# Optimization experiments

Hardware: AMD Instinct MI355X
Metric: run time of the kernel (lower is better)

The kernel has to match this reference:

```python
import jax, jax.numpy as jnp
import numpy as np

N = 50000
E = 1600000
D_IN = 512
EPS = 1e-5


def setup_inputs() -> dict:
    key = jax.random.key(0)
    ks = jax.random.split(key, 20)
    p = lambda k, shape: jax.random.normal(k, shape, dtype=jnp.float32) * 0.05
    return {
        "x": jax.random.normal(ks[0], (N, D_IN), dtype=jnp.float32),
        "edge_index": jax.random.randint(ks[1], (2, E), 0, N),
        "edge_weight": jax.random.uniform(ks[2], (E,), dtype=jnp.float32),
        # conv1: ChebConv(512->400) with K=1,2,3 (weight per Chebyshev order)
        "W1a": p(ks[3], (1, D_IN, 400)), "b1a": p(ks[4], (400,)),
        "W1b": p(ks[5], (2, D_IN, 400)), "b1b": p(ks[6], (400,)),
        "W1c": p(ks[7], (3, D_IN, 400)), "b1c": p(ks[8], (400,)),
        "g1": jnp.ones((1200,), jnp.float32), "beta1": jnp.zeros((1200,), jnp.float32),
        # conv2: ChebConv(1200->100) with K=1,2,3
        "W2a": p(ks[9], (1, 1200, 100)), "b2a": p(ks[10], (100,)),
        "W2b": p(ks[11], (2, 1200, 100)), "b2b": p(ks[12], (100,)),
        "W2c": p(ks[13], (3, 1200, 100)), "b2c": p(ks[14], (100,)),
        "g2": jnp.ones((300,), jnp.float32), "beta2": jnp.zeros((300,), jnp.float32),
        "Wl": p(ks[15], (300, 10)), "bl": p(ks[16], (10,)),
    }


def _cheb(x, row, col, norm, W, b):
    """PyG ChebConv forward: out = sum_k T_k(L_hat) x @ W[k] + b.
    L_hat (sym norm, lambda_max=2) = -D^{-1/2} A D^{-1/2}, zero diagonal,
    applied as scatter: (L_hat h)[col] += norm_e * h[row]."""
    K = W.shape[0]
    n = x.shape[0]
    prop = lambda h: jax.ops.segment_sum(norm[:, None] * h[row], col, num_segments=n)
    out = x @ W[0]
    Tx_prev, Tx = x, None
    if K >= 2:
        Tx = prop(x)
        out = out + Tx @ W[1]
    for k in range(2, K):
        Tx_new = 2.0 * prop(Tx) - Tx_prev
        out = out + Tx_new @ W[k]
        Tx_prev, Tx = Tx, Tx_new
    return out + b


def _bn(h, g, beta):
    # BatchNorm over nodes (training-mode batch statistics, biased var)
    mu = h.mean(axis=0)
    var = h.var(axis=0)
    return (h - mu) * jax.lax.rsqrt(var + EPS) * g + beta


def reference(x, edge_index, edge_weight, W1a, b1a, W1b, b1b, W1c, b1c, g1, beta1,
              W2a, b2a, W2b, b2b, W2c, b2c, g2, beta2, Wl, bl):
    row, col = edge_index[0], edge_index[1]
    deg = jax.ops.segment_sum(edge_weight, row, num_segments=x.shape[0])
    safe = jnp.where(deg > 0, deg, 1.0)
    dis = jnp.where(deg > 0, jax.lax.rsqrt(safe), 0.0)  # deg^{-1/2}, inf -> 0
    norm = -dis[row] * edge_weight * dis[col]  # scaled-Laplacian edge weights

    h = jnp.concatenate([
        _cheb(x, row, col, norm, W1a, b1a),
        _cheb(x, row, col, norm, W1b, b1b),
        _cheb(x, row, col, norm, W1c, b1c)], axis=1)  # [N, 1200]
    h = jax.nn.relu(_bn(h, g1, beta1))

    h = jnp.concatenate([
        _cheb(h, row, col, norm, W2a, b2a),
        _cheb(h, row, col, norm, W2b, b2b),
        _cheb(h, row, col, norm, W2c, b2c)], axis=1)  # [N, 300]
    h = _bn(h, g2, beta2)

    logits = h @ Wl + bl  # [N, 10]
    return jax.nn.log_softmax(logits, axis=1)
```

## Files before the change

### kernel.cpp

```cpp
#include <hip/hip_runtime.h>
#include <math.h>

#define EPSB 1e-5f

typedef __attribute__((ext_vector_type(8))) short short8;
typedef __attribute__((ext_vector_type(4))) float floatx4;
typedef __attribute__((ext_vector_type(2))) float floatx2;

__device__ inline float bf2f(unsigned short h) {
  union { unsigned int u; float f; } v; v.u = ((unsigned int)h) << 16; return v.f;
}
__device__ inline unsigned short f2bf(float f) {
  union { float f; unsigned int u; } v; v.f = f;
  unsigned int r = v.u + 0x7fffu + ((v.u >> 16) & 1u);
  return (unsigned short)(r >> 16);
}

__device__ __forceinline__ void gl2lds16(const unsigned short* g, unsigned short* l) {
  __builtin_amdgcn_global_load_lds(
      (const __attribute__((address_space(1))) unsigned int*)g,
      (__attribute__((address_space(3))) unsigned int*)l, 16, 0, 0);
}

__device__ __forceinline__ void pk4(floatx2* a, uint4 g, floatx2 wv) {
  unsigned int u[4] = {g.x, g.y, g.z, g.w};
#pragma unroll
  for (int j = 0; j < 4; j++) {
    union { unsigned int q; float f; } lo, hi;
    lo.q = u[j] << 16;
    hi.q = u[j] & 0xffff0000u;
    floatx2 v; v[0] = lo.f; v[1] = hi.f;
    asm("v_pk_fma_f32 %0, %1, %2, %0" : "+v"(a[j]) : "v"(v), "v"(wv));
  }
}


__global__ void degcnt_kernel(const int* __restrict__ row, const int* __restrict__ col,
                              const float* __restrict__ ew,
                              float* __restrict__ deg, int* __restrict__ cnt, int E) {
  int e = blockIdx.x * blockDim.x + threadIdx.x;
  if (e < E) {
    atomicAdd(&deg[row[e]], ew[e]);
    atomicAdd(&cnt[col[e]], 1);
  }
}

__global__ void dis_kernel(float* deg, int n) {
  int i = blockIdx.x * blockDim.x + threadIdx.x;
  if (i < n) { float d = deg[i]; deg[i] = d > 0.f ? rsqrtf(d) : 0.f; }
}

__global__ __launch_bounds__(1024) void scan1_kernel(const int* __restrict__ cnt,
                                                     int* __restrict__ off,
                                                     int* __restrict__ bsum, int n) {
  __shared__ int buf[1024];
  int tid = threadIdx.x;
  int idx = blockIdx.x * 1024 + tid;
  int v = (idx < n) ? cnt[idx] : 0;
  buf[tid] = v;
  __syncthreads();
  for (int s = 1; s < 1024; s <<= 1) {
    int t = (tid >= s) ? buf[tid - s] : 0;
    __syncthreads();
    if (tid >= s) buf[tid] += t;
    __syncthreads();
  }
  if (idx < n) off[idx] = buf[tid] - v;
  if (tid == 1023) bsum[blockIdx.x] = buf[1023];
}

__global__ void scan2_kernel(int* __restrict__ bsum, int* __restrict__ off,
                             int nb, int n) {
  if (threadIdx.x == 0 && blockIdx.x == 0) {
    int run = 0;
    for (int k = 0; k < nb; k++) { int t = bsum[k]; bsum[k] = run; run += t; }
    off[n] = run;
  }
}

__global__ void scan3_kernel(int* __restrict__ off, const int* __restrict__ bsum, int n) {
  int i = blockIdx.x * blockDim.x + threadIdx.x;
  if (i < n) off[i] += bsum[i >> 10];
}

__global__ void copy_kernel(const int* __restrict__ src, int* __restrict__ dst, int n) {
  int i = blockIdx.x * blockDim.x + threadIdx.x;
  if (i < n) dst[i] = src[i];
}

__global__ void fill_kernel(const int* __restrict__ row, const int* __restrict__ col,
                            const float* __restrict__ ew, const float* __restrict__ dis,
                            int* __restrict__ wptr,
                            int2* __restrict__ ePack, int E) {
  int e = blockIdx.x * blockDim.x + threadIdx.x;
  if (e < E) {
    int r = row[e], c = col[e];
    int p = atomicAdd(&wptr[c], 1);
    float nv = -dis[r] * ew[e] * dis[c];
    ePack[p] = make_int2(r, __float_as_int(nv));
  }
}


__global__ void cast_x_kernel(const float* __restrict__ x, unsigned short* __restrict__ xb,
                              int N) {
  int idx = blockIdx.x * blockDim.x + threadIdx.x;
  if (idx >= N * 128) return;
  int row = idx >> 7, c4 = idx & 127;
  float4 v = *reinterpret_cast<const float4*>(x + (size_t)row * 512 + c4 * 4);
  union { unsigned int u[2]; } p;
  p.u[0] = (unsigned int)f2bf(v.x) | ((unsigned int)f2bf(v.y) << 16);
  p.u[1] = (unsigned int)f2bf(v.z) | ((unsigned int)f2bf(v.w) << 16);
  *reinterpret_cast<uint2*>(xb + (size_t)row * 1536 + c4 * 4) = make_uint2(p.u[0], p.u[1]);
}

__global__ void wprep_kernel(const float* __restrict__ W, unsigned short* __restrict__ Bt,
                             int Ktot, int Nout, int ldBt, int rowOff) {
  int idx = blockIdx.x * blockDim.x + threadIdx.x;
  if (idx >= Ktot * Nout) return;
  int k = idx / Nout, n = idx - k * Nout;
  Bt[(size_t)(rowOff + n) * ldBt + k] = f2bf(W[idx]);
}

__global__ void padzero_kernel(unsigned short* __restrict__ h, int N) {
  int i = blockIdx.x * blockDim.x + threadIdx.x;
  if (i >= N * 2) return;
  *reinterpret_cast<uint4*>(h + (size_t)(i >> 1) * 1216 + 1200 + (i & 1) * 8) =
      make_uint4(0, 0, 0, 0);
}

__global__ void bcat_kernel(const float* __restrict__ a, const float* __restrict__ b,
                            const float* __restrict__ c, float* __restrict__ dst) {
  int i = threadIdx.x;
  if (i < 100) dst[i] = a[i];
  else if (i < 200) dst[i] = b[i - 100];
  else if (i < 300) dst[i] = c[i - 200];
}

__global__ __launch_bounds__(256) void prop_chunk_kernel(
    unsigned short* __restrict__ base, int ld,
    int srcCol, int dstCol, int subCol,
    const int* __restrict__ off, const int2* __restrict__ ePack,
    float scale, int N) {
  int chunk = blockIdx.x & 7;
  int g = blockIdx.x >> 3;
  int tid = threadIdx.x;
  int slot = (tid >> 3) & 3;
  int c8 = tid & 7;
  int v = g * 8 + (tid >> 5);
  bool valid = v < N;
  int vv = valid ? v : N - 1;
  int co = chunk * 64 + c8 * 8;
  const unsigned short* src = base + srcCol + co;
  int s = off[vv], e = off[vv + 1];
  int len = e - s;
  int s0 = s + (len * slot >> 2);
  int e0 = s + (len * (slot + 1) >> 2);
  floatx2 a2[4] = {}, b2[4] = {};
  int i = s0;
  for (; i + 3 < e0; i += 4) {
    int2 p0 = ePack[i];
    int2 p1 = ePack[i + 1];
    int2 p2 = ePack[i + 2];
    int2 p3 = ePack[i + 3];
    uint4 g0 = *reinterpret_cast<const uint4*>(src + (size_t)p0.x * ld);
    uint4 g1 = *reinterpret_cast<const uint4*>(src + (size_t)p1.x * ld);
    uint4 g2 = *reinterpret_cast<const uint4*>(src + (size_t)p2.x * ld);
    uint4 g3 = *reinterpret_cast<const uint4*>(src + (size_t)p3.x * ld);
    floatx2 w0; w0[0] = w0[1] = __int_as_float(p0.y);
    floatx2 w1; w1[0] = w1[1] = __int_as_float(p1.y);
    floatx2 w2; w2[0] = w2[1] = __int_as_float(p2.y);
    floatx2 w3; w3[0] = w3[1] = __int_as_float(p3.y);
    pk4(a2, g0, w0);
    pk4(b2, g1, w1);
    pk4(a2, g2, w2);
    pk4(b2, g3, w3);
  }
  for (; i < e0; i++) {
    int2 p = ePack[i];
    uint4 gg = *reinterpret_cast<const uint4*>(src + (size_t)p.x * ld);
    floatx2 wv; wv[0] = wv[1] = __int_as_float(p.y);
    pk4(a2, gg, wv);
  }
  float a[8];
#pragma unroll
  for (int j = 0; j < 4; j++) {
    a[2 * j]     = a2[j][0] + b2[j][0];
    a[2 * j + 1] = a2[j][1] + b2[j][1];
  }
#pragma unroll
  for (int j = 0; j < 8; j++) {
    a[j] += __shfl_xor(a[j], 8);
    a[j] += __shfl_xor(a[j], 16);
  }
  if (slot != 0 || !valid) return;
  if (subCol >= 0) {
    uint4 sv = *reinterpret_cast<const uint4*>(base + subCol + co + (size_t)v * ld);
    a[0] = scale * a[0] - bf2f((unsigned short)(sv.x & 0xffff));
    a[1] = scale * a[1] - bf2f((unsigned short)(sv.x >> 16));
    a[2] = scale * a[2] - bf2f((unsigned short)(sv.y & 0xffff));
    a[3] = scale * a[3] - bf2f((unsigned short)(sv.y >> 16));
    a[4] = scale * a[4] - bf2f((unsigned short)(sv.z & 0xffff));
    a[5] = scale * a[5] - bf2f((unsigned short)(sv.z >> 16));
    a[6] = scale * a[6] - bf2f((unsigned short)(sv.w & 0xffff));
    a[7] = scale * a[7] - bf2f((unsigned short)(sv.w >> 16));
  }
  uint4 o;
  o.x = (unsigned int)f2bf(a[0]) | ((unsigned int)f2bf(a[1]) << 16);
  o.y = (unsigned int)f2bf(a[2]) | ((unsigned int)f2bf(a[3]) << 16);
  o.z = (unsigned int)f2bf(a[4]) | ((unsigned int)f2bf(a[5]) << 16);
  o.w = (unsigned int)f2bf(a[6]) | ((unsigned int)f2bf(a[7]) << 16);
  *reinterpret_cast<uint4*>(base + dstCol + co + (size_t)v * ld) = o;
}

__global__ void prop_z_kernel(const unsigned short* __restrict__ Zcat,
                              const int* __restrict__ off, const int2* __restrict__ ePack,
                              float* __restrict__ h2f, unsigned short* __restrict__ U1) {
  int v = blockIdx.x;
  int f8 = threadIdx.x;
  if (f8 >= 38) return;
  int s = off[v], e = off[v + 1];
  floatx2 a2[4] = {}, b2[4] = {};
  int i = s;
  for (; i + 3 < e; i += 4) {
    int2 p0 = ePack[i];
    int2 p1 = ePack[i + 1];
    int2 p2 = ePack[i + 2];
    int2 p3 = ePack[i + 3];
    uint4 g0 = *reinterpret_cast<const uint4*>(Zcat + (size_t)p0.x * 304 + f8 * 8);
    uint4 g1 = *reinterpret_cast<const uint4*>(Zcat + (size_t)p1.x * 304 + f8 * 8);
    uint4 g2 = *reinterpret_cast<const uint4*>(Zcat + (size_t)p2.x * 304 + f8 * 8);
    uint4 g3 = *reinterpret_cast<const uint4*>(Zcat + (size_t)p3.x * 304 + f8 * 8);
    floatx2 w0; w0[0] = w0[1] = __int_as_float(p0.y);
    floatx2 w1; w1[0] = w1[1] = __int_as_float(p1.y);
    floatx2 w2; w2[0] = w2[1] = __int_as_float(p2.y);
    floatx2 w3; w3[0] = w3[1] = __int_as_float(p3.y);
    pk4(a2, g0, w0);
    pk4(b2, g1, w1);
    pk4(a2, g2, w2);
    pk4(b2, g3, w3);
  }
  for (; i < e; i++) {
    int2 p = ePack[i];
    uint4 raw = *reinterpret_cast<const uint4*>(Zcat + (size_t)p.x * 304 + f8 * 8);
    floatx2 wv; wv[0] = wv[1] = __int_as_float(p.y);
    pk4(a2, raw, wv);
  }
  float a[8];
#pragma unroll
  for (int j = 0; j < 4; j++) {
    a[2 * j]     = a2[j][0] + b2[j][0];
    a[2 * j + 1] = a2[j][1] + b2[j][1];
  }
  if (f8 < 25) {
    float* p = h2f + (size_t)v * 300 + 100 + f8 * 8;
#pragma unroll
    for (int j = 0; j < 8; j++) p[j] += a[j];
  } else {
    uint4 o;
    o.x = (unsigned int)f2bf(a[0]) | ((unsigned int)f2bf(a[1]) << 16);
    o.y = (unsigned int)f2bf(a[2]) | ((unsigned int)f2bf(a[3]) << 16);
    o.z = (unsigned int)f2bf(a[4]) | ((unsigned int)f2bf(a[5]) << 16);
    o.w = (unsigned int)f2bf(a[6]) | ((unsigned int)f2bf(a[7]) << 16);
    *reinterpret_cast<uint4*>(U1 + (size_t)v * 104 + (f8 - 25) * 8) = o;
  }
}

__global__ void prop_u_kernel(const unsigned short* __restrict__ U1,
                              const int* __restrict__ off, const int2* __restrict__ ePack,
                              const unsigned short* __restrict__ Zcat,
                              float* __restrict__ h2f) {
  int v = blockIdx.x;
  int f8 = threadIdx.x;
  if (f8 >= 13) return;
  int s = off[v], e = off[v + 1];
  floatx2 a2[4] = {}, b2[4] = {};
  int i = s;
  for (; i + 3 < e; i += 4) {
    int2 p0 = ePack[i];
    int2 p1 = ePack[i + 1];
    int2 p2 = ePack[i + 2];
    int2 p3 = ePack[i + 3];
    uint4 g0 = *reinterpret_cast<const uint4*>(U1 + (size_t)p0.x * 104 + f8 * 8);
    uint4 g1 = *reinterpret_cast<const uint4*>(U1 + (size_t)p1.x * 104 + f8 * 8);
    uint4 g2 = *reinterpret_cast<const uint4*>(U1 + (size_t)p2.x * 104 + f8 * 8);
    uint4 g3 = *reinterpret_cast<const uint4*>(U1 + (size_t)p3.x * 104 + f8 * 8);
    floatx2 w0; w0[0] = w0[1] = __int_as_float(p0.y);
    floatx2 w1; w1[0] = w1[1] = __int_as_float(p1.y);
    floatx2 w2; w2[0] = w2[1] = __int_as_float(p2.y);
    floatx2 w3; w3[0] = w3[1] = __int_as_float(p3.y);
    pk4(a2, g0, w0);
    pk4(b2, g1, w1);
    pk4(a2, g2, w2);
    pk4(b2, g3, w3);
  }
  for (; i < e; i++) {
    int2 p = ePack[i];
    uint4 raw = *reinterpret_cast<const uint4*>(U1 + (size_t)p.x * 104 + f8 * 8);
    floatx2 wv; wv[0] = wv[1] = __int_as_float(p.y);
    pk4(a2, raw, wv);
  }
  float a[8];
#pragma unroll
  for (int j = 0; j < 4; j++) {
    a[2 * j]     = a2[j][0] + b2[j][0];
    a[2 * j + 1] = a2[j][1] + b2[j][1];
  }
  const unsigned short* z2 = Zcat + (size_t)v * 304 + 200;
  float* p = h2f + (size_t)v * 300 + 200;
#pragma unroll
  for (int j = 0; j < 8; j++) {
    int c = f8 * 8 + j;
    if (c < 100) p[c] += 2.f * a[j] - bf2f(z2[c]);
  }
}

__global__ __launch_bounds__(256) void gemm_bf16_kernel(
    const unsigned short* __restrict__ A, int lda,
    const unsigned short* __restrict__ Bt, int ldb,
    int M, int Nc, int K,
    const float* __restrict__ bias,
    unsigned short* __restrict__ Cb, float* __restrict__ Cf, int ldc, int c0,
    int accumulate) {
  __shared__ __align__(16) unsigned short As[128 * 32];
  __shared__ __align__(16) unsigned short Bs[128 * 32];
  int tid = threadIdx.x;
  int wave = tid >> 6, lane = tid & 63;
  int q = lane >> 4, mn = lane & 15;
  int wr = wave >> 1, wc = wave & 1;
  int row0 = blockIdx.y * 128, col0 = blockIdx.x * 128;
  floatx4 acc[4][4] = {};

  const unsigned short* ga[2];
  const unsigned short* gb[2];
  unsigned short* la[2];
  unsigned short* lb[2];
#pragma unroll
  for (int j = 0; j < 2; j++) {
    int c = j * 256 + tid;
    int r = c >> 2, cw = (c & 3) * 8;
    int gr = row0 + r; if (gr > M - 1) gr = M - 1;
    ga[j] = A + (size_t)gr * lda + cw;
    int gn = col0 + r; if (gn > Nc - 1) gn = Nc - 1;
    gb[j] = Bt + (size_t)gn * ldb + cw;
    la[j] = &As[(j * 256 + wave * 64) * 8];
    lb[j] = &Bs[(j * 256 + wave * 64) * 8];
  }

  for (int k0 = 0; k0 < K; k0 += 32) {
#pragma unroll
    for (int j = 0; j < 2; j++) {
      gl2lds16(ga[j] + k0, la[j]);
      gl2lds16(gb[j] + k0, lb[j]);
    }
    __syncthreads();

    short8 af[4], bf[4];
#pragma unroll
    for (int i = 0; i < 4; i++) {
      af[i] = *reinterpret_cast<const short8*>(&As[(wr * 64 + i * 16 + mn) * 32 + q * 8]);
      bf[i] = *reinterpret_cast<const short8*>(&Bs[(wc * 64 + i * 16 + mn) * 32 + q * 8]);
    }
#pragma unroll
    for (int mi = 0; mi < 4; mi++)
#pragma unroll
      for (int ni = 0; ni < 4; ni++)
        acc[mi][ni] = __builtin_amdgcn_mfma_f32_16x16x32_bf16(af[mi], bf[ni], acc[mi][ni], 0, 0, 0);
    __syncthreads();
  }

#pragma unroll
  for (int mi = 0; mi < 4; mi++) {
#pragma unroll
    for (int ni = 0; ni < 4; ni++) {
      int gcol = col0 + wc * 64 + ni * 16 + mn;
      if (gcol >= Nc) continue;
      float b = bias ? bias[gcol] : 0.f;
#pragma unroll
      for (int r = 0; r < 4; r++) {
        int grow = row0 + wr * 64 + mi * 16 + q * 4 + r;
        if (grow >= M) continue;
        float v = acc[mi][ni][r] + b;
        if (Cb) {
          Cb[(size_t)grow * ldc + c0 + gcol] = f2bf(v);
        } else {
          float* p = Cf + (size_t)grow * ldc + c0 + gcol;
          if (accumulate) v += *p;
          *p = v;
        }
      }
    }
  }
}

__global__ void bn_stats_bf16_kernel(const unsigned short* __restrict__ h, int ld, int C,
                                     int N, float* __restrict__ sums) {
  int c = blockIdx.x * blockDim.x + threadIdx.x;
  if (c >= C) return;
  int r0 = blockIdx.y * 256;
  int r1 = min(N, r0 + 256);
  float s = 0.f, s2 = 0.f;
  for (int r = r0; r < r1; r++) {
    float v = bf2f(h[(size_t)r * ld + c]);
    s += v; s2 += v * v;
  }
  atomicAdd(&sums[c], s);
  atomicAdd(&sums[C + c], s2);
}

__global__ void scsh_kernel(const float* __restrict__ sums, const float* __restrict__ g,
                            const float* __restrict__ beta, float invN, int C,
                            float* __restrict__ scSh) {
  int c = blockIdx.x * blockDim.x + threadIdx.x;
  if (c >= C) return;
  float mu = sums[c] * invN;
  float var = sums[C + c] * invN - mu * mu;
  float s = rsqrtf(var + EPSB) * g[c];
  scSh[c] = s;
  scSh[C + c] = beta[c] - mu * s;
}

__global__ void bn_apply_bf16_kernel(unsigned short* __restrict__ h, int ld, int C8, int N,
                                     const float* __restrict__ scSh, int Cfull, int relu) {
  int idx = blockIdx.x * blockDim.x + threadIdx.x;
  if (idx >= N * C8) return;
  int row = idx / C8, c8 = idx - row * C8;
  unsigned short* p = h + (size_t)row * ld + c8 * 8;
  uint4 raw = *reinterpret_cast<uint4*>(p);
  float v[8];
  v[0] = bf2f((unsigned short)(raw.x & 0xffff)); v[1] = bf2f((unsigned short)(raw.x >> 16));
  v[2] = bf2f((unsigned short)(raw.y & 0xffff)); v[3] = bf2f((unsigned short)(raw.y >> 16));
  v[4] = bf2f((unsigned short)(raw.z & 0xffff)); v[5] = bf2f((unsigned short)(raw.z >> 16));
  v[6] = bf2f((unsigned short)(raw.w & 0xffff)); v[7] = bf2f((unsigned short)(raw.w >> 16));
#pragma unroll
  for (int j = 0; j < 8; j++) {
    int c = c8 * 8 + j;
    float o = v[j] * scSh[c] + scSh[Cfull + c];
    if (relu) o = fmaxf(o, 0.f);
    v[j] = o;
  }
  uint4 o;
  o.x = (unsigned int)f2bf(v[0]) | ((unsigned int)f2bf(v[1]) << 16);
  o.y = (unsigned int)f2bf(v[2]) | ((unsigned int)f2bf(v[3]) << 16);
  o.z = (unsigned int)f2bf(v[4]) | ((unsigned int)f2bf(v[5]) << 16);
  o.w = (unsigned int)f2bf(v[6]) | ((unsigned int)f2bf(v[7]) << 16);
  *reinterpret_cast<uint4*>(p) = o;
}

__global__ void bn_stats_kernel(const float* __restrict__ h, int C, int N,
                                float* __restrict__ sums) {
  int c = blockIdx.x * blockDim.x + threadIdx.x;
  if (c >= C) return;
  int r0 = blockIdx.y * 256;
  int r1 = min(N, r0 + 256);
  float s = 0.f, s2 = 0.f;
  for (int r = r0; r < r1; r++) {
    float v = h[(size_t)r * C + c];
    s += v; s2 += v * v;
  }
  atomicAdd(&sums[c], s);
  atomicAdd(&sums[C + c], s2);
}

__global__ void bn_apply_kernel(float* __restrict__ h, int C, int N,
                                const float* __restrict__ sums, const float* __restrict__ g,
                                const float* __restrict__ beta, float invN, int relu) {
  int C4 = C >> 2;
  int c4 = blockIdx.x * blockDim.x + threadIdx.x;
  if (c4 >= C4) return;
  float sc[4], sh[4];
#pragma unroll
  for (int j = 0; j < 4; j++) {
    int c = c4 * 4 + j;
    float mu = sums[c] * invN;
    float var = sums[C + c] * invN - mu * mu;
    float s = rsqrtf(var + EPSB) * g[c];
    sc[j] = s; sh[j] = beta[c] - mu * s;
  }
  int r0 = blockIdx.y * 256, r1 = min(N, r0 + 256);
  for (int r = r0; r < r1; r++) {
    float4* p = reinterpret_cast<float4*>(h + (size_t)r * C) + c4;
    float4 v = *p;
    v.x = v.x * sc[0] + sh[0]; v.y = v.y * sc[1] + sh[1];
    v.z = v.z * sc[2] + sh[2]; v.w = v.w * sc[3] + sh[3];
    if (relu) {
      v.x = fmaxf(v.x, 0.f); v.y = fmaxf(v.y, 0.f);
      v.z = fmaxf(v.z, 0.f); v.w = fmaxf(v.w, 0.f);
    }
    *p = v;
  }
}


__global__ __launch_bounds__(256) void final_bn_kernel(const float* __restrict__ h2,
                                                       const float* __restrict__ scSh,
                                                       const float* __restrict__ Wl,
                                                       const float* __restrict__ bl,
                                                       float* __restrict__ out, int N) {
  __shared__ float Ws[3000];
  __shared__ float S[600];
  for (int i = threadIdx.x; i < 3000; i += 256) Ws[i] = Wl[i];
  for (int i = threadIdx.x; i < 600; i += 256) S[i] = scSh[i];
  __syncthreads();
  int r = blockIdx.x * blockDim.x + threadIdx.x;
  if (r >= N) return;
  float acc[10];
#pragma unroll
  for (int c = 0; c < 10; c++) acc[c] = bl[c];
  const float* hr = h2 + (size_t)r * 300;
  for (int k = 0; k < 300; k++) {
    float x = hr[k] * S[k] + S[300 + k];
#pragma unroll
    for (int c = 0; c < 10; c++) acc[c] += x * Ws[k * 10 + c];
  }
  float mx = acc[0];
#pragma unroll
  for (int c = 1; c < 10; c++) mx = fmaxf(mx, acc[c]);
  float se = 0.f;
#pragma unroll
  for (int c = 0; c < 10; c++) se += expf(acc[c] - mx);
  float lz = mx + logf(se);
#pragma unroll
  for (int c = 0; c < 10; c++) out[(size_t)r * 10 + c] = acc[c] - lz;
}

__global__ __launch_bounds__(256) void final_kernel(const float* __restrict__ h2,
                                                    const float* __restrict__ Wl,
                                                    const float* __restrict__ bl,
                                                    float* __restrict__ out, int N) {
  __shared__ float Ws[3000];
  for (int i = threadIdx.x; i < 3000; i += 256) Ws[i] = Wl[i];
  __syncthreads();
  int r = blockIdx.x * blockDim.x + threadIdx.x;
  if (r >= N) return;
  float acc[10];
#pragma unroll
  for (int c = 0; c < 10; c++) acc[c] = bl[c];
  const float* hr = h2 + (size_t)r * 300;
  for (int k = 0; k < 300; k++) {
    float x = hr[k];
#pragma unroll
    for (int c = 0; c < 10; c++) acc[c] += x * Ws[k * 10 + c];
  }
  float mx = acc[0];
#pragma unroll
  for (int c = 1; c < 10; c++) mx = fmaxf(mx, acc[c]);
  float se = 0.f;
#pragma unroll
  for (int c = 0; c < 10; c++) se += expf(acc[c] - mx);
  float lz = mx + logf(se);
#pragma unroll
  for (int c = 0; c < 10; c++) out[(size_t)r * 10 + c] = acc[c] - lz;
}


__global__ void prop_kernel(const float* __restrict__ src, int srcLd4, int D4,
                            const int* __restrict__ off, const int2* __restrict__ ePack,
                            float* __restrict__ dst, int dstLd4,
                            const float* __restrict__ sub, int subLd4, float scale) {
  int v = blockIdx.x;
  int f4 = threadIdx.x;
  if (f4 >= D4) return;
  int s = off[v], e = off[v + 1];
  float ax = 0.f, ay = 0.f, az = 0.f, aw = 0.f;
  for (int i = s; i < e; i++) {
    int2 p = ePack[i];
    float w = __int_as_float(p.y);
    const float4 hv = *reinterpret_cast<const float4*>(src + ((size_t)p.x * srcLd4 + f4) * 4);
    ax += w * hv.x; ay += w * hv.y; az += w * hv.z; aw += w * hv.w;
  }
  float4 o;
  if (sub) {
    const float4 sv = *reinterpret_cast<const float4*>(sub + ((size_t)v * subLd4 + f4) * 4);
    o.x = scale * ax - sv.x; o.y = scale * ay - sv.y;
    o.z = scale * az - sv.z; o.w = scale * aw - sv.w;
  } else {
    o.x = ax; o.y = ay; o.z = az; o.w = aw;
  }
  *reinterpret_cast<float4*>(dst + ((size_t)v * dstLd4 + f4) * 4) = o;
}

#define BM 64
#define BN 64
#define BK 16

__global__ __launch_bounds__(256) void gemm_kernel(
    const float* __restrict__ A, int lda,
    const float* __restrict__ B, int ldb,
    float* __restrict__ C, int ldc, int c0,
    int M, int Nc, int K,
    const float* __restrict__ bias, int accumulate) {
  __shared__ float As[BK][BM + 4];
  __shared__ float Bs[BK][BN + 4];
  int tid = threadIdx.x;
  int tx = tid & 15, ty = tid >> 4;
  int row0 = blockIdx.y * BM, col0 = blockIdx.x * BN;
  float acc[4][4] = {};
  int aM = tid >> 2;
  int aK = (tid & 3) << 2;
  int bK = tid >> 4;
  int bN = (tid & 15) << 2;
  for (int k0 = 0; k0 < K; k0 += BK) {
    float4 av = make_float4(0.f, 0.f, 0.f, 0.f);
    int ar = row0 + aM;
    if (ar < M && k0 + aK < K)
      av = *reinterpret_cast<const float4*>(A + (size_t)ar * lda + k0 + aK);
    As[aK + 0][aM] = av.x; As[aK + 1][aM] = av.y;
    As[aK + 2][aM] = av.z; As[aK + 3][aM] = av.w;
    float4 bv = make_float4(0.f, 0.f, 0.f, 0.f);
    int bc = col0 + bN;
    if (bc < Nc && k0 + bK < K)
      bv = *reinterpret_cast<const float4*>(B + (size_t)(k0 + bK) * ldb + bc);
    Bs[bK][bN + 0] = bv.x; Bs[bK][bN + 1] = bv.y;
    Bs[bK][bN + 2] = bv.z; Bs[bK][bN + 3] = bv.w;
    __syncthreads();
#pragma unroll
    for (int k = 0; k < BK; k++) {
      float a0 = As[k][ty * 4 + 0], a1 = As[k][ty * 4 + 1];
      float a2 = As[k][ty * 4 + 2], a3 = As[k][ty * 4 + 3];
      float b0 = Bs[k][tx * 4 + 0], b1 = Bs[k][tx * 4 + 1];
      float b2 = Bs[k][tx * 4 + 2], b3 = Bs[k][tx * 4 + 3];
      acc[0][0] += a0 * b0; acc[0][1] += a0 * b1; acc[0][2] += a0 * b2; acc[0][3] += a0 * b3;
      acc[1][0] += a1 * b0; acc[1][1] += a1 * b1; acc[1][2] += a1 * b2; acc[1][3] += a1 * b3;
      acc[2][0] += a2 * b0; acc[2][1] += a2 * b1; acc[2][2] += a2 * b2; acc[2][3] += a2 * b3;
      acc[3][0] += a3 * b0; acc[3][1] += a3 * b1; acc[3][2] += a3 * b2; acc[3][3] += a3 * b3;
    }
    __syncthreads();
  }
#pragma unroll
  for (int i = 0; i < 4; i++) {
    int r = row0 + ty * 4 + i;
    if (r >= M) continue;
#pragma unroll
    for (int j = 0; j < 4; j++) {
      int c = col0 + tx * 4 + j;
      if (c >= Nc) continue;
      float v = acc[i][j];
      if (bias) v += bias[c];
      float* p = C + (size_t)r * ldc + c0 + c;
      if (accumulate) *p += v; else *p = v;
    }
  }
}


extern "C" void kernel_launch(void* const* d_in, const int* in_sizes, int n_in,
                              void* d_out, int out_size, void* d_ws, size_t ws_size,
                              hipStream_t stream) {
  const float* x   = (const float*)d_in[0];
  const int*   ei  = (const int*)d_in[1];
  const float* ew  = (const float*)d_in[2];
  const float* W1a = (const float*)d_in[3];
  const float* b1a = (const float*)d_in[4];
  const float* W1b = (const float*)d_in[5];
  const float* b1b = (const float*)d_in[6];
  const float* W1c = (const float*)d_in[7];
  const float* b1c = (const float*)d_in[8];
  const float* g1  = (const float*)d_in[9];
  const float* be1 = (const float*)d_in[10];
  const float* W2a = (const float*)d_in[11];
  const float* b2a = (const float*)d_in[12];
  const float* W2b = (const float*)d_in[13];
  const float* b2b = (const float*)d_in[14];
  const float* W2c = (const float*)d_in[15];
  const float* b2c = (const float*)d_in[16];
  const float* g2  = (const float*)d_in[17];
  const float* be2 = (const float*)d_in[18];
  const float* Wl  = (const float*)d_in[19];
  const float* bl  = (const float*)d_in[20];
  float* out = (float*)d_out;

  const int N = in_sizes[0] / 512;
  const int E = in_sizes[1] / 2;
  const int* row = ei;
  const int* col = ei + E;
  (void)n_in; (void)out_size;

  int eb = (E + 255) / 256;
  int nb = (N + 255) / 256;
  int nb1 = (N + 1023) / 1024;

  char* ws = (char*)d_ws;
  size_t o = 0;
  int2*  ePack = (int2*)(ws + o);  o += (size_t)E * 8;
  float* dis   = (float*)(ws + o); o += (size_t)N * 4;
  int*   cnt   = (int*)(ws + o);   o += (size_t)N * 4;
  int*   off   = (int*)(ws + o);   o += (size_t)(N + 4) * 4;
  int*   wptr  = (int*)(ws + o);   o += (size_t)N * 4;
  int*   bsum  = (int*)(ws + o);   o += (size_t)(nb1 + 4) * 4;
  float* sums  = (float*)(ws + o); o += 2400 * 4;
  float* scSh  = (float*)(ws + o); o += 2400 * 4;
  float* bcat  = (float*)(ws + o); o += 304 * 4;
  o = (o + 255) & ~(size_t)255;
  size_t oCommon = o;

  size_t oA = oCommon;
  unsigned short* Bt1a = (unsigned short*)(ws + oA); oA += (size_t)400 * 512 * 2;
  unsigned short* Bt1b = (unsigned short*)(ws + oA); oA += (size_t)400 * 1024 * 2;
  unsigned short* Bt1c = (unsigned short*)(ws + oA); oA += (size_t)400 * 1536 * 2;
  unsigned short* Bt2cat0 = (unsigned short*)(ws + oA); oA += (size_t)304 * 1216 * 2;
  unsigned short* Bt2z    = (unsigned short*)(ws + oA); oA += (size_t)304 * 1216 * 2;
  oA = (oA + 255) & ~(size_t)255;
  unsigned short* h1n = (unsigned short*)(ws + oA); oA += (size_t)N * 1216 * 2;
  oA = (oA + 255) & ~(size_t)255;
  float* h2f = (float*)(ws + oA); oA += (size_t)N * 300 * 4;
  oA = (oA + 255) & ~(size_t)255;
  unsigned short* Xcat = (unsigned short*)(ws + oA); oA += (size_t)N * 1536 * 2;
  unsigned short* Zcat = Xcat;
  unsigned short* U1 = Xcat + (size_t)N * 304;

  bool planA = (ws_size >= oA);

  hipMemsetAsync(dis, 0, (size_t)N * 4, stream);
  hipMemsetAsync(cnt, 0, (size_t)N * 4, stream);
  degcnt_kernel<<<eb, 256, 0, stream>>>(row, col, ew, dis, cnt, E);
  dis_kernel<<<nb, 256, 0, stream>>>(dis, N);
  scan1_kernel<<<nb1, 1024, 0, stream>>>(cnt, off, bsum, N);
  scan2_kernel<<<1, 64, 0, stream>>>(bsum, off, nb1, N);
  scan3_kernel<<<nb, 256, 0, stream>>>(off, bsum, N);
  copy_kernel<<<nb, 256, 0, stream>>>(off, wptr, N);
  fill_kernel<<<eb, 256, 0, stream>>>(row, col, ew, dis, wptr, ePack, E);

  if (planA) {
    wprep_kernel<<<(400 * 512 + 255) / 256, 256, 0, stream>>>(W1a, Bt1a, 512, 400, 512, 0);
    wprep_kernel<<<(400 * 1024 + 255) / 256, 256, 0, stream>>>(W1b, Bt1b, 1024, 400, 1024, 0);
    wprep_kernel<<<(400 * 1536 + 255) / 256, 256, 0, stream>>>(W1c, Bt1c, 1536, 400, 1536, 0);
    hipMemsetAsync(Bt2cat0, 0, (size_t)304 * 1216 * 2, stream);
    hipMemsetAsync(Bt2z, 0, (size_t)304 * 1216 * 2, stream);
    wprep_kernel<<<(100 * 1200 + 255) / 256, 256, 0, stream>>>(W2a, Bt2cat0, 1200, 100, 1216, 0);
    wprep_kernel<<<(100 * 1200 + 255) / 256, 256, 0, stream>>>(W2b, Bt2cat0, 1200, 100, 1216, 100);
    wprep_kernel<<<(100 * 1200 + 255) / 256, 256, 0, stream>>>(W2c, Bt2cat0, 1200, 100, 1216, 200);
    wprep_kernel<<<(100 * 1200 + 255) / 256, 256, 0, stream>>>(W2b + 1200 * 100, Bt2z, 1200, 100, 1216, 0);
    wprep_kernel<<<(100 * 1200 + 255) / 256, 256, 0, stream>>>(W2c + 1200 * 100, Bt2z, 1200, 100, 1216, 100);
    wprep_kernel<<<(100 * 1200 + 255) / 256, 256, 0, stream>>>(W2c + 2 * 1200 * 100, Bt2z, 1200, 100, 1216, 200);
    bcat_kernel<<<1, 320, 0, stream>>>(b2a, b2b, b2c, bcat);
    cast_x_kernel<<<(N * 128 + 255) / 256, 256, 0, stream>>>(x, Xcat, N);
    padzero_kernel<<<(N * 2 + 255) / 256, 256, 0, stream>>>(h1n, N);

    int gridP = ((N + 7) / 8) * 8;
    prop_chunk_kernel<<<gridP, 256, 0, stream>>>(Xcat, 1536, 0, 512, -1,
                                                 off, ePack, 1.f, N);
    prop_chunk_kernel<<<gridP, 256, 0, stream>>>(Xcat, 1536, 512, 1024, 0,
                                                 off, ePack, 2.f, N);

    dim3 gA((400 + 127) / 128, (N + 127) / 128);
    gemm_bf16_kernel<<<gA, 256, 0, stream>>>(Xcat, 1536, Bt1a, 512, N, 400, 512,
                                             b1a, h1n, nullptr, 1216, 0, 0);
    gemm_bf16_kernel<<<gA, 256, 0, stream>>>(Xcat, 1536, Bt1b, 1024, N, 400, 1024,
                                             b1b, h1n, nullptr, 1216, 400, 0);
    gemm_bf16_kernel<<<gA, 256, 0, stream>>>(Xcat, 1536, Bt1c, 1536, N, 400, 1536,
                                             b1c, h1n, nullptr, 1216, 800, 0);

    hipMemsetAsync(sums, 0, 2400 * 4, stream);
    dim3 s1g((1200 + 255) / 256, (N + 255) / 256);
    bn_stats_bf16_kernel<<<s1g, 256, 0, stream>>>(h1n, 1216, 1200, N, sums);
    scsh_kernel<<<(1200 + 255) / 256, 256, 0, stream>>>(sums, g1, be1, 1.f / (float)N, 1200, scSh);
    bn_apply_bf16_kernel<<<((size_t)N * 150 + 255) / 256, 256, 0, stream>>>(
        h1n, 1216, 150, N, scSh, 1200, 1);

    dim3 gB0((300 + 127) / 128, (N + 127) / 128);
    gemm_bf16_kernel<<<gB0, 256, 0, stream>>>(h1n, 1216, Bt2cat0, 1216, N, 300, 1216,
                                              bcat, nullptr, h2f, 300, 0, 0);

    dim3 gBz((304 + 127) / 128, (N + 127) / 128);
    gemm_bf16_kernel<<<gBz, 256, 0, stream>>>(h1n, 1216, Bt2z, 1216, N, 304, 1216,
                                              nullptr, Zcat, nullptr, 304, 0, 0);

    prop_z_kernel<<<N, 64, 0, stream>>>(Zcat, off, ePack, h2f, U1);
    prop_u_kernel<<<N, 64, 0, stream>>>(U1, off, ePack, Zcat, h2f);

    hipMemsetAsync(sums, 0, 2400 * 4, stream);
    dim3 s2g((300 + 255) / 256, (N + 255) / 256);
    bn_stats_kernel<<<s2g, 256, 0, stream>>>(h2f, 300, N, sums);
    scsh_kernel<<<(300 + 255) / 256, 256, 0, stream>>>(sums, g2, be2, 1.f / (float)N, 300, scSh);
    final_bn_kernel<<<nb, 256, 0, stream>>>(h2f, scSh, Wl, bl, out, N);
    return;
  }

  size_t oB = oCommon;
  float* h2 = (float*)(ws + oB); oB += (size_t)N * 300 * 4;
  oB = (oB + 255) & ~(size_t)255;
  float* h1 = (float*)(ws + oB); oB += (size_t)N * 1200 * 4;
  oB = (oB + 255) & ~(size_t)255;
  size_t avail = (ws_size > oB) ? (ws_size - oB) : 0;
  int C1 = 64;
  { const int opts[4] = {512, 256, 128, 64};
    for (int i = 0; i < 4; i++)
      if ((size_t)2 * N * opts[i] * 4 <= avail) { C1 = opts[i]; break; } }
  int C2 = 100;
  { const int opts[6] = {1200, 600, 400, 300, 200, 100};
    for (int i = 0; i < 6; i++)
      if ((size_t)2 * N * opts[i] * 4 <= avail) { C2 = opts[i]; break; } }
  int maxC = C1 > C2 ? C1 : C2;
  float* S1 = (float*)(ws + oB);
  float* S2 = S1 + (size_t)N * maxC;

  dim3 g1d((400 + BN - 1) / BN, (N + BM - 1) / BM);
  gemm_kernel<<<g1d, 256, 0, stream>>>(x, 512, W1a, 400, h1, 1200, 0,   N, 400, 512, b1a, 0);
  gemm_kernel<<<g1d, 256, 0, stream>>>(x, 512, W1b, 400, h1, 1200, 400, N, 400, 512, b1b, 0);
  gemm_kernel<<<g1d, 256, 0, stream>>>(x, 512, W1c, 400, h1, 1200, 800, N, 400, 512, b1c, 0);
  for (int c = 0; c < 512; c += C1) {
    int D4 = C1 / 4;
    int bt = ((D4 + 63) / 64) * 64;
    prop_kernel<<<N, bt, 0, stream>>>(x + c, 128, D4, off, ePack, S1, D4, nullptr, 0, 1.f);
    gemm_kernel<<<g1d, 256, 0, stream>>>(S1, C1, W1b + (size_t)(512 + c) * 400, 400, h1, 1200, 400, N, 400, C1, nullptr, 1);
    gemm_kernel<<<g1d, 256, 0, stream>>>(S1, C1, W1c + (size_t)(512 + c) * 400, 400, h1, 1200, 800, N, 400, C1, nullptr, 1);
    prop_kernel<<<N, bt, 0, stream>>>(S1, D4, D4, off, ePack, S2, D4, x + c, 128, 2.f);
    gemm_kernel<<<g1d, 256, 0, stream>>>(S2, C1, W1c + (size_t)(2 * 512 + c) * 400, 400, h1, 1200, 800, N, 400, C1, nullptr, 1);
  }

  hipMemsetAsync(sums, 0, 2400 * 4, stream);
  dim3 s1g((1200 + 255) / 256, (N + 255) / 256);
  bn_stats_kernel<<<s1g, 256, 0, stream>>>(h1, 1200, N, sums);
  dim3 a1g((300 + 63) / 64, (N + 255) / 256);
  bn_apply_kernel<<<a1g, 64, 0, stream>>>(h1, 1200, N, sums, g1, be1, 1.f / (float)N, 1);

  dim3 g2d((100 + BN - 1) / BN, (N + BM - 1) / BM);
  gemm_kernel<<<g2d, 256, 0, stream>>>(h1, 1200, W2a, 100, h2, 300, 0,   N, 100, 1200, b2a, 0);
  gemm_kernel<<<g2d, 256, 0, stream>>>(h1, 1200, W2b, 100, h2, 300, 100, N, 100, 1200, b2b, 0);
  gemm_kernel<<<g2d, 256, 0, stream>>>(h1, 1200, W2c, 100, h2, 300, 200, N, 100, 1200, b2c, 0);
  for (int c = 0; c < 1200; c += C2) {
    int D4 = C2 / 4;
    int bt = ((D4 + 63) / 64) * 64;
    prop_kernel<<<N, bt, 0, stream>>>(h1 + c, 300, D4, off, ePack, S1, D4, nullptr, 0, 1.f);
    gemm_kernel<<<g2d, 256, 0, stream>>>(S1, C2, W2b + (size_t)(1200 + c) * 100, 100, h2, 300, 100, N, 100, C2, nullptr, 1);
    gemm_kernel<<<g2d, 256, 0, stream>>>(S1, C2, W2c + (size_t)(1200 + c) * 100, 100, h2, 300, 200, N, 100, C2, nullptr, 1);
    prop_kernel<<<N, bt, 0, stream>>>(S1, D4, D4, off, ePack, S2, D4, h1 + c, 300, 2.f);
    gemm_kernel<<<g2d, 256, 0, stream>>>(S2, C2, W2c + (size_t)(2 * 1200 + c) * 100, 100, h2, 300, 200, N, 100, C2, nullptr, 1);
  }

  hipMemsetAsync(sums, 0, 2400 * 4, stream);
  dim3 s2g((300 + 255) / 256, (N + 255) / 256);
  bn_stats_kernel<<<s2g, 256, 0, stream>>>(h2, 300, N, sums);
  dim3 a2g((75 + 63) / 64, (N + 255) / 256);
  bn_apply_kernel<<<a2g, 64, 0, stream>>>(h2, 300, N, sums, g2, be2, 1.f / (float)N, 0);

  final_kernel<<<nb, 256, 0, stream>>>(h2, Wl, bl, out, N);
}
```

Baseline: 1.853 ms.

## Precompute byte offsets per edge and assign one node per thread group in propagation

The fill kernel now writes three more packed edge arrays. Each holds the source row already multiplied by the byte stride of its target matrix, so the gather loops skip the 64-bit index multiply. prop_chunk_kernel drops the four-way split of each node's edge list across slots and the shuffle reduction. Each 8-thread group now handles a whole node, 32 nodes per block, with a quarter of the previous grid. In exchange the fill pass writes three more E-sized arrays, and load balance gets worse for high-degree nodes because fewer threads share each edge list.

```diff
diff --git a/kernel.cpp b/kernel.cpp
--- a/kernel.cpp
+++ b/kernel.cpp
@@ -91,13 +91,18 @@
 __global__ void fill_kernel(const int* __restrict__ row, const int* __restrict__ col,
                             const float* __restrict__ ew, const float* __restrict__ dis,
                             int* __restrict__ wptr,
-                            int2* __restrict__ ePack, int E) {
+                            int2* __restrict__ ePack, int2* __restrict__ eA,
+                            int2* __restrict__ eZ, int2* __restrict__ eU, int E) {
   int e = blockIdx.x * blockDim.x + threadIdx.x;
   if (e < E) {
     int r = row[e], c = col[e];
     int p = atomicAdd(&wptr[c], 1);
     float nv = -dis[r] * ew[e] * dis[c];
-    ePack[p] = make_int2(r, __float_as_int(nv));
+    int wb = __float_as_int(nv);
+    ePack[p] = make_int2(r, wb);
+    eA[p] = make_int2(r * 3072, wb);
+    eZ[p] = make_int2(r * 608, wb);
+    eU[p] = make_int2(r * 208, wb);
   }
 }
 
@@ -140,33 +145,29 @@
 __global__ __launch_bounds__(256) void prop_chunk_kernel(
     unsigned short* __restrict__ base, int ld,
     int srcCol, int dstCol, int subCol,
-    const int* __restrict__ off, const int2* __restrict__ ePack,
+    const int* __restrict__ off, const int2* __restrict__ eA,
     float scale, int N) {
   int chunk = blockIdx.x & 7;
   int g = blockIdx.x >> 3;
   int tid = threadIdx.x;
-  int slot = (tid >> 3) & 3;
   int c8 = tid & 7;
-  int v = g * 8 + (tid >> 5);
+  int v = g * 32 + (tid >> 3);
   bool valid = v < N;
   int vv = valid ? v : N - 1;
   int co = chunk * 64 + c8 * 8;
-  const unsigned short* src = base + srcCol + co;
+  const char* src = (const char*)(base + srcCol + co);
   int s = off[vv], e = off[vv + 1];
-  int len = e - s;
-  int s0 = s + (len * slot >> 2);
-  int e0 = s + (len * (slot + 1) >> 2);
   floatx2 a2[4] = {}, b2[4] = {};
-  int i = s0;
-  for (; i + 3 < e0; i += 4) {
-    int2 p0 = ePack[i];
-    int2 p1 = ePack[i + 1];
-    int2 p2 = ePack[i + 2];
-    int2 p3 = ePack[i + 3];
-    uint4 g0 = *reinterpret_cast<const uint4*>(src + (size_t)p0.x * ld);
-    uint4 g1 = *reinterpret_cast<const uint4*>(src + (size_t)p1.x * ld);
-    uint4 g2 = *reinterpret_cast<const uint4*>(src + (size_t)p2.x * ld);
-    uint4 g3 = *reinterpret_cast<const uint4*>(src + (size_t)p3.x * ld);
+  int i = s;
+  for (; i + 3 < e; i += 4) {
+    int2 p0 = eA[i];
+    int2 p1 = eA[i + 1];
+    int2 p2 = eA[i + 2];
+    int2 p3 = eA[i + 3];
+    uint4 g0 = *reinterpret_cast<const uint4*>(src + (unsigned)p0.x);
+    uint4 g1 = *reinterpret_cast<const uint4*>(src + (unsigned)p1.x);
+    uint4 g2 = *reinterpret_cast<const uint4*>(src + (unsigned)p2.x);
+    uint4 g3 = *reinterpret_cast<const uint4*>(src + (unsigned)p3.x);
     floatx2 w0; w0[0] = w0[1] = __int_as_float(p0.y);
     floatx2 w1; w1[0] = w1[1] = __int_as_float(p1.y);
     floatx2 w2; w2[0] = w2[1] = __int_as_float(p2.y);
@@ -176,24 +177,19 @@
     pk4(a2, g2, w2);
     pk4(b2, g3, w3);
   }
-  for (; i < e0; i++) {
-    int2 p = ePack[i];
-    uint4 gg = *reinterpret_cast<const uint4*>(src + (size_t)p.x * ld);
+  for (; i < e; i++) {
+    int2 p = eA[i];
+    uint4 gg = *reinterpret_cast<const uint4*>(src + (unsigned)p.x);
     floatx2 wv; wv[0] = wv[1] = __int_as_float(p.y);
     pk4(a2, gg, wv);
   }
+  if (!valid) return;
   float a[8];
 #pragma unroll
   for (int j = 0; j < 4; j++) {
     a[2 * j]     = a2[j][0] + b2[j][0];
     a[2 * j + 1] = a2[j][1] + b2[j][1];
   }
-#pragma unroll
-  for (int j = 0; j < 8; j++) {
-    a[j] += __shfl_xor(a[j], 8);
-    a[j] += __shfl_xor(a[j], 16);
-  }
-  if (slot != 0 || !valid) return;
   if (subCol >= 0) {
     uint4 sv = *reinterpret_cast<const uint4*>(base + subCol + co + (size_t)v * ld);
     a[0] = scale * a[0] - bf2f((unsigned short)(sv.x & 0xffff));
@@ -214,23 +210,24 @@
 }
 
 __global__ void prop_z_kernel(const unsigned short* __restrict__ Zcat,
-                              const int* __restrict__ off, const int2* __restrict__ ePack,
+                              const int* __restrict__ off, const int2* __restrict__ eZ,
                               float* __restrict__ h2f, unsigned short* __restrict__ U1) {
   int v = blockIdx.x;
   int f8 = threadIdx.x;
   if (f8 >= 38) return;
   int s = off[v], e = off[v + 1];
+  const char* srcB = (const char*)Zcat + f8 * 16;
   floatx2 a2[4] = {}, b2[4] = {};
   int i = s;
   for (; i + 3 < e; i += 4) {
-    int2 p0 = ePack[i];
-    int2 p1 = ePack[i + 1];
-    int2 p2 = ePack[i + 2];
-    int2 p3 = ePack[i + 3];
-    uint4 g0 = *reinterpret_cast<const uint4*>(Zcat + (size_t)p0.x * 304 + f8 * 8);
-    uint4 g1 = *reinterpret_cast<const uint4*>(Zcat + (size_t)p1.x * 304 + f8 * 8);
-    uint4 g2 = *reinterpret_cast<const uint4*>(Zcat + (size_t)p2.x * 304 + f8 * 8);
-    uint4 g3 = *reinterpret_cast<const uint4*>(Zcat + (size_t)p3.x * 304 + f8 * 8);
+    int2 p0 = eZ[i];
+    int2 p1 = eZ[i + 1];
+    int2 p2 = eZ[i + 2];
+    int2 p3 = eZ[i + 3];
+    uint4 g0 = *reinterpret_cast<const uint4*>(srcB + (unsigned)p0.x);
+    uint4 g1 = *reinterpret_cast<const uint4*>(srcB + (unsigned)p1.x);
+    uint4 g2 = *reinterpret_cast<const uint4*>(srcB + (unsigned)p2.x);
+    uint4 g3 = *reinterpret_cast<const uint4*>(srcB + (unsigned)p3.x);
     floatx2 w0; w0[0] = w0[1] = __int_as_float(p0.y);
     floatx2 w1; w1[0] = w1[1] = __int_as_float(p1.y);
     floatx2 w2; w2[0] = w2[1] = __int_as_float(p2.y);
@@ -241,8 +238,8 @@
     pk4(b2, g3, w3);
   }
   for (; i < e; i++) {
-    int2 p = ePack[i];
-    uint4 raw = *reinterpret_cast<const uint4*>(Zcat + (size_t)p.x * 304 + f8 * 8);
+    int2 p = eZ[i];
+    uint4 raw = *reinterpret_cast<const uint4*>(srcB + (unsigned)p.x);
     floatx2 wv; wv[0] = wv[1] = __int_as_float(p.y);
     pk4(a2, raw, wv);
   }
@@ -267,24 +264,25 @@
 }
 
 __global__ void prop_u_kernel(const unsigned short* __restrict__ U1,
-                              const int* __restrict__ off, const int2* __restrict__ ePack,
+                              const int* __restrict__ off, const int2* __restrict__ eU,
                               const unsigned short* __restrict__ Zcat,
                               float* __restrict__ h2f) {
   int v = blockIdx.x;
   int f8 = threadIdx.x;
   if (f8 >= 13) return;
   int s = off[v], e = off[v + 1];
+  const char* srcB = (const char*)U1 + f8 * 16;
   floatx2 a2[4] = {}, b2[4] = {};
   int i = s;
   for (; i + 3 < e; i += 4) {
-    int2 p0 = ePack[i];
-    int2 p1 = ePack[i + 1];
-    int2 p2 = ePack[i + 2];
-    int2 p3 = ePack[i + 3];
-    uint4 g0 = *reinterpret_cast<const uint4*>(U1 + (size_t)p0.x * 104 + f8 * 8);
-    uint4 g1 = *reinterpret_cast<const uint4*>(U1 + (size_t)p1.x * 104 + f8 * 8);
-    uint4 g2 = *reinterpret_cast<const uint4*>(U1 + (size_t)p2.x * 104 + f8 * 8);
-    uint4 g3 = *reinterpret_cast<const uint4*>(U1 + (size_t)p3.x * 104 + f8 * 8);
+    int2 p0 = eU[i];
+    int2 p1 = eU[i + 1];
+    int2 p2 = eU[i + 2];
+    int2 p3 = eU[i + 3];
+    uint4 g0 = *reinterpret_cast<const uint4*>(srcB + (unsigned)p0.x);
+    uint4 g1 = *reinterpret_cast<const uint4*>(srcB + (unsigned)p1.x);
+    uint4 g2 = *reinterpret_cast<const uint4*>(srcB + (unsigned)p2.x);
+    uint4 g3 = *reinterpret_cast<const uint4*>(srcB + (unsigned)p3.x);
     floatx2 w0; w0[0] = w0[1] = __int_as_float(p0.y);
     floatx2 w1; w1[0] = w1[1] = __int_as_float(p1.y);
     floatx2 w2; w2[0] = w2[1] = __int_as_float(p2.y);
@@ -295,8 +293,8 @@
     pk4(b2, g3, w3);
   }
   for (; i < e; i++) {
-    int2 p = ePack[i];
-    uint4 raw = *reinterpret_cast<const uint4*>(U1 + (size_t)p.x * 104 + f8 * 8);
+    int2 p = eU[i];
+    uint4 raw = *reinterpret_cast<const uint4*>(srcB + (unsigned)p.x);
     floatx2 wv; wv[0] = wv[1] = __int_as_float(p.y);
     pk4(a2, raw, wv);
   }
@@ -683,6 +681,9 @@
   char* ws = (char*)d_ws;
   size_t o = 0;
   int2*  ePack = (int2*)(ws + o);  o += (size_t)E * 8;
+  int2*  eA    = (int2*)(ws + o);  o += (size_t)E * 8;
+  int2*  eZ    = (int2*)(ws + o);  o += (size_t)E * 8;
+  int2*  eU    = (int2*)(ws + o);  o += (size_t)E * 8;
   float* dis   = (float*)(ws + o); o += (size_t)N * 4;
   int*   cnt   = (int*)(ws + o);   o += (size_t)N * 4;
   int*   off   = (int*)(ws + o);   o += (size_t)(N + 4) * 4;
@@ -719,7 +720,7 @@
   scan2_kernel<<<1, 64, 0, stream>>>(bsum, off, nb1, N);
   scan3_kernel<<<nb, 256, 0, stream>>>(off, bsum, N);
   copy_kernel<<<nb, 256, 0, stream>>>(off, wptr, N);
-  fill_kernel<<<eb, 256, 0, stream>>>(row, col, ew, dis, wptr, ePack, E);
+  fill_kernel<<<eb, 256, 0, stream>>>(row, col, ew, dis, wptr, ePack, eA, eZ, eU, E);
 
   if (planA) {
     wprep_kernel<<<(400 * 512 + 255) / 256, 256, 0, stream>>>(W1a, Bt1a, 512, 400, 512, 0);
@@ -737,11 +738,11 @@
     cast_x_kernel<<<(N * 128 + 255) / 256, 256, 0, stream>>>(x, Xcat, N);
     padzero_kernel<<<(N * 2 + 255) / 256, 256, 0, stream>>>(h1n, N);
 
-    int gridP = ((N + 7) / 8) * 8;
+    int gridP = ((N + 31) / 32) * 8;
     prop_chunk_kernel<<<gridP, 256, 0, stream>>>(Xcat, 1536, 0, 512, -1,
-                                                 off, ePack, 1.f, N);
+                                                 off, eA, 1.f, N);
     prop_chunk_kernel<<<gridP, 256, 0, stream>>>(Xcat, 1536, 512, 1024, 0,
-                                                 off, ePack, 2.f, N);
+                                                 off, eA, 2.f, N);
 
     dim3 gA((400 + 127) / 128, (N + 127) / 128);
     gemm_bf16_kernel<<<gA, 256, 0, stream>>>(Xcat, 1536, Bt1a, 512, N, 400, 512,
@@ -766,8 +767,8 @@
     gemm_bf16_kernel<<<gBz, 256, 0, stream>>>(h1n, 1216, Bt2z, 1216, N, 304, 1216,
                                               nullptr, Zcat, nullptr, 304, 0, 0);
 
-    prop_z_kernel<<<N, 64, 0, stream>>>(Zcat, off, ePack, h2f, U1);
-    prop_u_kernel<<<N, 64, 0, stream>>>(U1, off, ePack, Zcat, h2f);
+    prop_z_kernel<<<N, 64, 0, stream>>>(Zcat, off, eZ, h2f, U1);
+    prop_u_kernel<<<N, 64, 0, stream>>>(U1, off, eU, Zcat, h2f);
 
     hipMemsetAsync(sums, 0, 2400 * 4, stream);
     dim3 s2g((300 + 255) / 256, (N + 255) / 256);
```

Result: slower. 1.919 ms (+3.6%).
